# Kernel optimization log

Hardware: AMD Instinct MI355X
Metric: run time of the kernel (lower is better)

## Reference

```python
import jax, jax.numpy as jnp
import numpy as np

E, K, H, I = 8, 2, 768, 1152  # experts, top_k, hidden, intermediate
T = 4096  # total tokens


def setup_inputs() -> dict:
    key = jax.random.key(0)
    ks = jax.random.split(key, 6)
    return {
        "x": jax.random.normal(ks[0], (T, H), jnp.float32),
        "gate_w": jax.random.normal(ks[1], (E, H), jnp.float32) * 0.02,
        "correction_bias": jnp.zeros((E,), jnp.float32),
        "Wi": jax.random.normal(ks[2], (E, H, 2 * I), jnp.float32) * 0.02,
        "Wo": jax.random.normal(ks[3], (E, I, H), jnp.float32) * 0.02,
        "shared_Wi": jax.random.normal(ks[4], (2 * I, H), jnp.float32) * 0.02,
        "shared_Wo": jax.random.normal(ks[5], (H, I), jnp.float32) * 0.02,
    }


def reference(x, gate_w, correction_bias, Wi, Wo, shared_Wi, shared_Wo):
    # ---- shared SwiGLU expert (dropout=0 in eval) ----
    sh = x @ shared_Wi.T                      # (T, 2I)
    s_in, s_gate = sh[:, :I], sh[:, I:]
    shared_out = (jax.nn.silu(s_in) * s_gate) @ shared_Wo.T  # (T, H)

    # ---- sigmoid top-k router with bias correction ----
    logits = jax.nn.sigmoid(x @ gate_w.T)     # (T, E)
    sel = logits + correction_bias
    _, indices = jax.lax.top_k(sel, K)        # (T, K)
    weights = jnp.take_along_axis(logits, indices, axis=-1)  # bias-free scores
    weights = weights / jnp.sum(weights, axis=-1, keepdims=True)

    # combine weight per (expert, token): cw[e, t] = sum_k weights[t,k]*[indices[t,k]==e]
    one_hot = jax.nn.one_hot(indices, E, dtype=x.dtype)      # (T, K, E)
    cw = jnp.einsum("tke,tk->et", one_hot, weights)          # (E, T)

    # ---- experts: SwiGLU per expert, weighted scatter-combine ----
    h = jnp.einsum("th,ehf->etf", x, Wi)      # (E, T, 2I)
    proj, gate = h[..., :I], h[..., I:]
    act = jax.nn.silu(gate) * proj            # (E, T, I)
    act = act * cw[:, :, None]                # fold combine weights before Wo
    expert_out = jnp.einsum("eti,eih->th", act, Wo)          # (T, H)

    return expert_out + shared_out
```

## Files before the change

### kernel.cpp

```cpp
#include <hip/hip_runtime.h>
#include <stdint.h>

#define E_  8
#define H_  768
#define I_  1152
#define T_  4096
#define F2_ (2*I_)

typedef unsigned short u16;
typedef __attribute__((ext_vector_type(8))) __bf16 bf16x8;
typedef __attribute__((ext_vector_type(4))) float floatx4;

typedef const void __attribute__((address_space(1))) as1_void;
typedef void __attribute__((address_space(3))) as3_void;

__device__ __forceinline__ void gld16(void* lds, const void* g) {
  __builtin_amdgcn_global_load_lds((as1_void*)g, (as3_void*)lds, 16, 0, 0);
}

__device__ __forceinline__ u16 f2bf(float f) {
  union { float f; unsigned int i; } v; v.f = f;
  unsigned int r = v.i + 0x7FFF + ((v.i >> 16) & 1);
  return (u16)(r >> 16);
}

__global__ void convert_two(const float* __restrict__ s1, u16* __restrict__ d1, int n1,
                            const float* __restrict__ s2, u16* __restrict__ d2) {
  int i = (blockIdx.x * 256 + threadIdx.x) * 4;
  const float* s; u16* d;
  if (i < n1) { s = s1 + i; d = d1 + i; }
  else        { s = s2 + (i - n1); d = d2 + (i - n1); }
  float4 v = *(const float4*)s;
  ushort4 u;
  u.x = f2bf(v.x); u.y = f2bf(v.y); u.z = f2bf(v.z); u.w = f2bf(v.w);
  *(ushort4*)d = u;
}

__global__ void transpose_f2b(const float* __restrict__ src, u16* __restrict__ dst,
                              int R, int C) {
  __shared__ u16 tile[64][65];
  const float* s = src + (long)blockIdx.z * R * C;
  u16*         d = dst + (long)blockIdx.z * R * C;
  int r0 = blockIdx.y * 64, c0 = blockIdx.x * 64;
  int tx = threadIdx.x, ty = threadIdx.y;
  #pragma unroll
  for (int k = 0; k < 64; k += 8)
    tile[ty + k][tx] = f2bf(s[(long)(r0 + ty + k) * C + (c0 + tx)]);
  __syncthreads();
  #pragma unroll
  for (int k = 0; k < 64; k += 8)
    d[(long)(c0 + ty + k) * R + (r0 + tx)] = tile[tx][ty + k];
}

__global__ void gate_kernel(const float* __restrict__ x, const float* __restrict__ gw,
                            const float* __restrict__ bias,
                            int* __restrict__ top2e, float* __restrict__ top2w,
                            u16* __restrict__ xb) {
  int t    = blockIdx.x * 4 + (threadIdx.x >> 6);
  int lane = threadIdx.x & 63;
  float acc[E_];
  #pragma unroll
  for (int e = 0; e < E_; e++) acc[e] = 0.f;
  #pragma unroll
  for (int i = 0; i < H_ / 256; i++) {
    int c = i * 256 + lane * 4;
    float4 xv = *(const float4*)(x + (long)t * H_ + c);
    ushort4 u;
    u.x = f2bf(xv.x); u.y = f2bf(xv.y); u.z = f2bf(xv.z); u.w = f2bf(xv.w);
    *(ushort4*)(xb + (long)t * H_ + c) = u;
    #pragma unroll
    for (int e = 0; e < E_; e++) {
      float4 g = *(const float4*)(gw + e * H_ + c);
      acc[e] += xv.x * g.x + xv.y * g.y + xv.z * g.z + xv.w * g.w;
    }
  }
  #pragma unroll
  for (int e = 0; e < E_; e++) {
    #pragma unroll
    for (int s = 32; s > 0; s >>= 1) acc[e] += __shfl_xor(acc[e], s);
  }
  if (lane == 0) {
    float logits[E_], sel[E_];
    #pragma unroll
    for (int e = 0; e < E_; e++) {
      logits[e] = 1.f / (1.f + expf(-acc[e]));
      sel[e]    = logits[e] + bias[e];
    }
    int i0 = 0;
    #pragma unroll
    for (int e = 1; e < E_; e++) if (sel[e] > sel[i0]) i0 = e;
    int i1 = (i0 == 0) ? 1 : 0;
    #pragma unroll
    for (int e = 0; e < E_; e++) if (e != i0 && sel[e] > sel[i1]) i1 = e;
    float w0 = logits[i0], w1 = logits[i1], s = w0 + w1;
    top2e[t * 2 + 0] = i0;  top2w[t * 2 + 0] = w0 / s;
    top2e[t * 2 + 1] = i1;  top2w[t * 2 + 1] = w1 / s;
  }
}

__global__ void build_lists(const int* __restrict__ top2e, const float* __restrict__ top2w,
                            int* __restrict__ counts, int* __restrict__ offs,
                            int* __restrict__ list, float* __restrict__ wlist,
                            int* __restrict__ pos) {
  __shared__ int scnt[4][E_];
  __shared__ int sq[4];
  __shared__ int soffs[E_];
  int e = blockIdx.x;
  int tid = threadIdx.x, w = tid >> 6, lane = tid & 63;
  const int Q = (2 * T_) / 4;

  int c8[E_];
  #pragma unroll
  for (int q = 0; q < E_; q++) c8[q] = 0;
  for (int i = tid; i < 2 * T_; i += 256) {
    int v = top2e[i];
    #pragma unroll
    for (int q = 0; q < E_; q++) c8[q] += (v == q);
  }
  int qstart = w * Q;
  int ce = 0;
  for (int i = qstart + lane; i < qstart + Q; i += 64) ce += (top2e[i] == e);
  #pragma unroll
  for (int q = 0; q < E_; q++)
    #pragma unroll
    for (int s = 32; s > 0; s >>= 1) c8[q] += __shfl_xor(c8[q], s);
  #pragma unroll
  for (int s = 32; s > 0; s >>= 1) ce += __shfl_xor(ce, s);
  if (lane == 0) {
    #pragma unroll
    for (int q = 0; q < E_; q++) scnt[w][q] = c8[q];
    sq[w] = ce;
  }
  __syncthreads();
  if (tid == 0) {
    int s = 0;
    #pragma unroll
    for (int q = 0; q < E_; q++) {
      int tot = scnt[0][q] + scnt[1][q] + scnt[2][q] + scnt[3][q];
      soffs[q] = s;
      if (e == 0) { counts[q] = tot; offs[q] = s; }
      s += tot;
    }
    if (e == 0) { counts[8] = T_; offs[8] = 2 * T_; }
  }
  __syncthreads();
  int base = soffs[e];
  #pragma unroll
  for (int w2 = 0; w2 < 4; w2++) if (w2 < w) base += sq[w2];
  unsigned long long lt = (lane == 63) ? (~0ull >> 1) : ((1ull << lane) - 1);
  for (int i0 = qstart; i0 < qstart + Q; i0 += 64) {
    int s = i0 + lane;
    bool m = (top2e[s] == e);
    unsigned long long mask = __ballot(m);
    if (m) {
      int p = base + __popcll(mask & lt);
      list[p]  = s >> 1;
      wlist[p] = top2w[s];
      pos[s]   = p;
    }
    base += __popcll(mask);
  }
  for (int t = e * (T_ / 8) + tid; t < (e + 1) * (T_ / 8); t += 256) {
    list[2 * T_ + t]  = t;
    wlist[2 * T_ + t] = 1.f;
  }
}

#define PP1 168
__global__ __launch_bounds__(256, 2)
void gemm_act_all(const u16* __restrict__ A, const u16* __restrict__ WiT,
                  const u16* __restrict__ sWib, u16* __restrict__ act,
                  const int* __restrict__ list, const float* __restrict__ wlist,
                  const int* __restrict__ counts, const int* __restrict__ offsets) {
  __shared__ __align__(16) u16 As[128 * 64];
  __shared__ __align__(16) u16 Bs[2][64 * 64];

  int id = blockIdx.x;
  int y  = id / PP1, p = id - y * PP1;
  if (p >= 162) return;
  int z = p / 18, xblk = p - z * 18;

  int cnt = counts[z], off = offsets[z];
  int row0 = y * 128;
  if (row0 >= cnt) return;
  const u16* B = (z == 8) ? sWib : (WiT + (long)z * F2_ * H_);
  int n0 = xblk * 64;

  int tid  = threadIdx.x;
  int lane = tid & 63, wv = tid >> 6;
  int wr   = wv >> 1, wc = wv & 1;
  int half = lane & 15, quad = lane >> 4;

  int rA  = tid >> 3;
  int lc8 = ((tid & 7) ^ (rA & 7)) * 8;
  const u16* ap[4];
  #pragma unroll
  for (int n = 0; n < 4; n++) {
    int rr = min(row0 + rA + n * 32, cnt - 1);
    ap[n] = A + (long)list[off + rr] * H_ + lc8;
  }
  const u16* bp[2][2];
  #pragma unroll
  for (int h = 0; h < 2; h++)
    #pragma unroll
    for (int m = 0; m < 2; m++)
      bp[h][m] = B + (long)(h * I_ + n0 + m * 32 + rA) * H_ + lc8;

  floatx4 acc[2][4][2];
  #pragma unroll
  for (int q = 0; q < 2; q++)
    #pragma unroll
    for (int i = 0; i < 4; i++)
      #pragma unroll
      for (int j = 0; j < 2; j++) acc[q][i][j] = (floatx4)0.f;

  for (int k0 = 0; k0 < H_; k0 += 64) {
    if (k0) __syncthreads();
    #pragma unroll
    for (int n = 0; n < 4; n++) gld16(As + (n * 256 + tid) * 8, ap[n] + k0);
    #pragma unroll
    for (int h = 0; h < 2; h++)
      #pragma unroll
      for (int m = 0; m < 2; m++) gld16(Bs[h] + (m * 256 + tid) * 8, bp[h][m] + k0);
    __syncthreads();
    #pragma unroll
    for (int kk = 0; kk < 2; kk++) {
      int cs = ((kk * 4 + quad) ^ (half & 7)) * 8;
      bf16x8 a[4], bq[2][2];
      #pragma unroll
      for (int i = 0; i < 4; i++)
        a[i] = *(const bf16x8*)(As + (wr * 64 + i * 16 + half) * 64 + cs);
      #pragma unroll
      for (int q = 0; q < 2; q++)
        #pragma unroll
        for (int j = 0; j < 2; j++)
          bq[q][j] = *(const bf16x8*)(Bs[q] + (wc * 32 + j * 16 + half) * 64 + cs);
      #pragma unroll
      for (int i = 0; i < 4; i++)
        #pragma unroll
        for (int q = 0; q < 2; q++)
          #pragma unroll
          for (int j = 0; j < 2; j++)
            acc[q][i][j] = __builtin_amdgcn_mfma_f32_16x16x32_bf16(a[i], bq[q][j], acc[q][i][j], 0, 0, 0);
    }
  }

  bool sh = (z == 8);
  #pragma unroll
  for (int i = 0; i < 4; i++) {
    #pragma unroll
    for (int r = 0; r < 4; r++) {
      int g = row0 + wr * 64 + i * 16 + quad * 4 + r;
      if (g < cnt) {
        float w = wlist[off + g];
        #pragma unroll
        for (int j = 0; j < 2; j++) {
          float va = acc[0][i][j][r];
          float vb = acc[1][i][j][r];
          float zz = sh ? va : vb;
          float o  = sh ? vb : va;
          float sg = zz / (1.f + expf(-zz));
          float v  = sg * o * w;
          int col  = n0 + wc * 32 + j * 16 + half;
          act[(long)(off + g) * I_ + col] = f2bf(v);
        }
      }
    }
  }
}

#define PP2 56
__global__ __launch_bounds__(256, 2)
void gemm_out_all(const u16* __restrict__ A, const u16* __restrict__ WoT,
                  const u16* __restrict__ sWob, float* __restrict__ out,
                  float* __restrict__ eobuf,
                  const int* __restrict__ counts, const int* __restrict__ offsets) {
  __shared__ __align__(16) u16 As[128 * 64];
  __shared__ __align__(16) u16 Bs[128 * 64];

  int id = blockIdx.x;
  int y  = id / PP2, p = id - y * PP2;
  if (p >= 54) return;
  int z = p / 6, xblk = p - z * 6;

  int cnt = counts[z], off = offsets[z];
  int row0 = y * 128;
  if (row0 >= cnt) return;
  const u16* B = (z == 8) ? sWob : (WoT + (long)z * H_ * I_);
  int n0 = xblk * 128;

  int tid  = threadIdx.x;
  int lane = tid & 63, wv = tid >> 6;
  int wr   = wv >> 1, wc = wv & 1;
  int half = lane & 15, quad = lane >> 4;

  int rA  = tid >> 3;
  int lc8 = ((tid & 7) ^ (rA & 7)) * 8;
  const u16* ap[4];
  #pragma unroll
  for (int n = 0; n < 4; n++) {
    long rr = off + min(row0 + rA + n * 32, cnt - 1);
    ap[n] = A + rr * I_ + lc8;
  }
  const u16* bp[4];
  #pragma unroll
  for (int m = 0; m < 4; m++)
    bp[m] = B + (long)(n0 + m * 32 + rA) * I_ + lc8;

  floatx4 acc[4][4];
  #pragma unroll
  for (int i = 0; i < 4; i++)
    #pragma unroll
    for (int j = 0; j < 4; j++) acc[i][j] = (floatx4)0.f;

  for (int k0 = 0; k0 < I_; k0 += 64) {
    if (k0) __syncthreads();
    #pragma unroll
    for (int n = 0; n < 4; n++) gld16(As + (n * 256 + tid) * 8, ap[n] + k0);
    #pragma unroll
    for (int m = 0; m < 4; m++) gld16(Bs + (m * 256 + tid) * 8, bp[m] + k0);
    __syncthreads();
    #pragma unroll
    for (int kk = 0; kk < 2; kk++) {
      int cs = ((kk * 4 + quad) ^ (half & 7)) * 8;
      bf16x8 a[4], b[4];
      #pragma unroll
      for (int i = 0; i < 4; i++)
        a[i] = *(const bf16x8*)(As + (wr * 64 + i * 16 + half) * 64 + cs);
      #pragma unroll
      for (int j = 0; j < 4; j++)
        b[j] = *(const bf16x8*)(Bs + (wc * 64 + j * 16 + half) * 64 + cs);
      #pragma unroll
      for (int i = 0; i < 4; i++)
        #pragma unroll
        for (int j = 0; j < 4; j++)
          acc[i][j] = __builtin_amdgcn_mfma_f32_16x16x32_bf16(a[i], b[j], acc[i][j], 0, 0, 0);
    }
  }

  bool sh = (z == 8);
  #pragma unroll
  for (int i = 0; i < 4; i++) {
    #pragma unroll
    for (int r = 0; r < 4; r++) {
      int g = row0 + wr * 64 + i * 16 + quad * 4 + r;
      if (g < cnt) {
        float* orow = sh ? (out + (long)g * H_) : (eobuf + (long)(off + g) * H_);
        #pragma unroll
        for (int j = 0; j < 4; j++) {
          int col = n0 + wc * 64 + j * 16 + half;
          orow[col] = acc[i][j][r];
        }
      }
    }
  }
}

__global__ void final_reduce(float* __restrict__ out, const float* __restrict__ eobuf,
                             const int* __restrict__ pos) {
  int gid = blockIdx.x * 256 + threadIdx.x;
  int t = gid / (H_ / 4), c = (gid % (H_ / 4)) * 4;
  int p0 = pos[t * 2], p1 = pos[t * 2 + 1];
  float4 a = *(const float4*)(out   + (long)t  * H_ + c);
  float4 b = *(const float4*)(eobuf + (long)p0 * H_ + c);
  float4 d = *(const float4*)(eobuf + (long)p1 * H_ + c);
  a.x += b.x + d.x; a.y += b.y + d.y; a.z += b.z + d.z; a.w += b.w + d.w;
  *(float4*)(out + (long)t * H_ + c) = a;
}

extern "C" void kernel_launch(void* const* d_in, const int* in_sizes, int n_in,
                              void* d_out, int out_size, void* d_ws, size_t ws_size,
                              hipStream_t stream) {
  const float* x      = (const float*)d_in[0];
  const float* gate_w = (const float*)d_in[1];
  const float* bias   = (const float*)d_in[2];
  const float* Wi     = (const float*)d_in[3];
  const float* Wo     = (const float*)d_in[4];
  const float* sWi    = (const float*)d_in[5];
  const float* sWo    = (const float*)d_in[6];
  float* out          = (float*)d_out;

  char* ws = (char*)d_ws;
  size_t o = 0;
  auto alloc = [&](size_t bytes) -> void* {
    o = (o + 255) & ~(size_t)255;
    void* p = ws + o;
    o += bytes;
    return p;
  };
  u16*   xb    = (u16*)  alloc((size_t)T_ * H_ * 2);
  u16*   sWib  = (u16*)  alloc((size_t)F2_ * H_ * 2);
  u16*   sWob  = (u16*)  alloc((size_t)H_ * I_ * 2);
  u16*   WiT   = (u16*)  alloc((size_t)E_ * F2_ * H_ * 2);
  u16*   WoT   = (u16*)  alloc((size_t)E_ * H_ * I_ * 2);
  u16*   act   = (u16*)  alloc((size_t)3 * T_ * I_ * 2);
  int*   top2e = (int*)  alloc((size_t)T_ * 2 * 4);
  float* top2w = (float*)alloc((size_t)T_ * 2 * 4);
  int*   count = (int*)  alloc(9 * 4);
  int*   offs  = (int*)  alloc(9 * 4);
  int*   list  = (int*)  alloc((size_t)3 * T_ * 4);
  float* wlist = (float*)alloc((size_t)3 * T_ * 4);
  int*   pos   = (int*)  alloc((size_t)2 * T_ * 4);
  float* eobuf = (float*)WiT;

  gate_kernel<<<T_ / 4, 256, 0, stream>>>(x, gate_w, bias, top2e, top2w, xb);
  build_lists<<<E_, 256, 0, stream>>>(top2e, top2w, count, offs, list, wlist, pos);

  convert_two<<<(F2_ * H_ + H_ * I_) / 1024, 256, 0, stream>>>(
      sWi, sWib, F2_ * H_, sWo, sWob);
  transpose_f2b<<<dim3(F2_ / 64, H_ / 64, E_), dim3(64, 8), 0, stream>>>(Wi, WiT, H_, F2_);
  transpose_f2b<<<dim3(H_ / 64, I_ / 64, E_), dim3(64, 8), 0, stream>>>(Wo, WoT, I_, H_);

  gemm_act_all<<<32 * PP1, 256, 0, stream>>>(xb, WiT, sWib, act, list, wlist, count, offs);
  gemm_out_all<<<32 * PP2, 256, 0, stream>>>(act, WoT, sWob, out, eobuf, count, offs);
  final_reduce<<<(T_ * (H_ / 4)) / 256, 256, 0, stream>>>(out, eobuf, pos);
}
```

Measured before the change: 300.2 us.

## Double-buffer LDS tiles in both expert GEMM kernels to overlap loads with MFMA

Both grouped GEMM kernels now use two LDS buffers for the A and B tiles. The async global-to-LDS loads for the next K-slab are issued before the MFMA work on the current slab, and there is one barrier per slab instead of two. The aim is to hide global memory latency behind compute. In exchange, LDS use per block doubles, which could limit occupancy, and each barrier still waits for all outstanding loads to finish.

```diff
diff --git a/kernel.cpp b/kernel.cpp
--- a/kernel.cpp
+++ b/kernel.cpp
@@ -172,8 +172,10 @@
                   const u16* __restrict__ sWib, u16* __restrict__ act,
                   const int* __restrict__ list, const float* __restrict__ wlist,
                   const int* __restrict__ counts, const int* __restrict__ offsets) {
-  __shared__ __align__(16) u16 As[128 * 64];
-  __shared__ __align__(16) u16 Bs[2][64 * 64];
+  __shared__ __align__(16) u16 As0[128 * 64];
+  __shared__ __align__(16) u16 As1[128 * 64];
+  __shared__ __align__(16) u16 Bs0[2 * 64 * 64];
+  __shared__ __align__(16) u16 Bs1[2 * 64 * 64];
 
   int id = blockIdx.x;
   int y  = id / PP1, p = id - y * PP1;
@@ -214,27 +216,28 @@
       #pragma unroll
       for (int j = 0; j < 2; j++) acc[q][i][j] = (floatx4)0.f;
 
-  for (int k0 = 0; k0 < H_; k0 += 64) {
-    if (k0) __syncthreads();
-    #pragma unroll
-    for (int n = 0; n < 4; n++) gld16(As + (n * 256 + tid) * 8, ap[n] + k0);
-    #pragma unroll
-    for (int h = 0; h < 2; h++)
-      #pragma unroll
-      for (int m = 0; m < 2; m++) gld16(Bs[h] + (m * 256 + tid) * 8, bp[h][m] + k0);
-    __syncthreads();
+  auto stage = [&](u16* as, u16* bs, int k0) {
+    #pragma unroll
+    for (int n = 0; n < 4; n++) gld16(as + (n * 256 + tid) * 8, ap[n] + k0);
+    #pragma unroll
+    for (int h2 = 0; h2 < 2; h2++)
+      #pragma unroll
+      for (int m = 0; m < 2; m++)
+        gld16(bs + h2 * 4096 + (m * 256 + tid) * 8, bp[h2][m] + k0);
+  };
+  auto compute = [&](const u16* as, const u16* bs) {
     #pragma unroll
     for (int kk = 0; kk < 2; kk++) {
       int cs = ((kk * 4 + quad) ^ (half & 7)) * 8;
       bf16x8 a[4], bq[2][2];
       #pragma unroll
       for (int i = 0; i < 4; i++)
-        a[i] = *(const bf16x8*)(As + (wr * 64 + i * 16 + half) * 64 + cs);
+        a[i] = *(const bf16x8*)(as + (wr * 64 + i * 16 + half) * 64 + cs);
       #pragma unroll
       for (int q = 0; q < 2; q++)
         #pragma unroll
         for (int j = 0; j < 2; j++)
-          bq[q][j] = *(const bf16x8*)(Bs[q] + (wc * 32 + j * 16 + half) * 64 + cs);
+          bq[q][j] = *(const bf16x8*)(bs + q * 4096 + (wc * 32 + j * 16 + half) * 64 + cs);
       #pragma unroll
       for (int i = 0; i < 4; i++)
         #pragma unroll
@@ -243,6 +246,17 @@
           for (int j = 0; j < 2; j++)
             acc[q][i][j] = __builtin_amdgcn_mfma_f32_16x16x32_bf16(a[i], bq[q][j], acc[q][i][j], 0, 0, 0);
     }
+  };
+
+  stage(As0, Bs0, 0);
+  __syncthreads();
+  for (int k0 = 0; k0 < H_; k0 += 128) {
+    stage(As1, Bs1, k0 + 64);
+    compute(As0, Bs0);
+    __syncthreads();
+    if (k0 + 128 < H_) stage(As0, Bs0, k0 + 128);
+    compute(As1, Bs1);
+    if (k0 + 128 < H_) __syncthreads();
   }
 
   bool sh = (z == 8);
@@ -275,8 +289,10 @@
                   const u16* __restrict__ sWob, float* __restrict__ out,
                   float* __restrict__ eobuf,
                   const int* __restrict__ counts, const int* __restrict__ offsets) {
-  __shared__ __align__(16) u16 As[128 * 64];
-  __shared__ __align__(16) u16 Bs[128 * 64];
+  __shared__ __align__(16) u16 As0[128 * 64];
+  __shared__ __align__(16) u16 As1[128 * 64];
+  __shared__ __align__(16) u16 Bs0[128 * 64];
+  __shared__ __align__(16) u16 Bs1[128 * 64];
 
   int id = blockIdx.x;
   int y  = id / PP2, p = id - y * PP2;
@@ -313,29 +329,40 @@
     #pragma unroll
     for (int j = 0; j < 4; j++) acc[i][j] = (floatx4)0.f;
 
-  for (int k0 = 0; k0 < I_; k0 += 64) {
-    if (k0) __syncthreads();
-    #pragma unroll
-    for (int n = 0; n < 4; n++) gld16(As + (n * 256 + tid) * 8, ap[n] + k0);
-    #pragma unroll
-    for (int m = 0; m < 4; m++) gld16(Bs + (m * 256 + tid) * 8, bp[m] + k0);
-    __syncthreads();
+  auto stage = [&](u16* as, u16* bs, int k0) {
+    #pragma unroll
+    for (int n = 0; n < 4; n++) gld16(as + (n * 256 + tid) * 8, ap[n] + k0);
+    #pragma unroll
+    for (int m = 0; m < 4; m++) gld16(bs + (m * 256 + tid) * 8, bp[m] + k0);
+  };
+  auto compute = [&](const u16* as, const u16* bs) {
     #pragma unroll
     for (int kk = 0; kk < 2; kk++) {
       int cs = ((kk * 4 + quad) ^ (half & 7)) * 8;
       bf16x8 a[4], b[4];
       #pragma unroll
       for (int i = 0; i < 4; i++)
-        a[i] = *(const bf16x8*)(As + (wr * 64 + i * 16 + half) * 64 + cs);
+        a[i] = *(const bf16x8*)(as + (wr * 64 + i * 16 + half) * 64 + cs);
       #pragma unroll
       for (int j = 0; j < 4; j++)
-        b[j] = *(const bf16x8*)(Bs + (wc * 64 + j * 16 + half) * 64 + cs);
+        b[j] = *(const bf16x8*)(bs + (wc * 64 + j * 16 + half) * 64 + cs);
       #pragma unroll
       for (int i = 0; i < 4; i++)
         #pragma unroll
         for (int j = 0; j < 4; j++)
           acc[i][j] = __builtin_amdgcn_mfma_f32_16x16x32_bf16(a[i], b[j], acc[i][j], 0, 0, 0);
     }
+  };
+
+  stage(As0, Bs0, 0);
+  __syncthreads();
+  for (int k0 = 0; k0 < I_; k0 += 128) {
+    stage(As1, Bs1, k0 + 64);
+    compute(As0, Bs0);
+    __syncthreads();
+    if (k0 + 128 < I_) stage(As0, Bs0, k0 + 128);
+    compute(As1, Bs1);
+    if (k0 + 128 < I_) __syncthreads();
   }
 
   bool sh = (z == 8);
```

New measurement: 306.7 us. 1.02x slower.

## Fuse prep kernels into one launch, reorder GEMM block mapping, shrink out-GEMM tile

Applied to the files above, without the earlier changes.

Merges the gate/routing, shared-weight conversion and the two expert weight transposes into one prep_all kernel that dispatches on block index. This removes three launches and lets independent prep work share the GPU. Both GEMMs now put the row-block index in the low bits of the block id, so consecutive blocks share the same weight columns. gemm_out_all uses 64-row tiles with occupancy hint 4, which doubles its grid for better load balance at the cost of more reloads of the B tiles.

```diff
diff --git a/kernel.cpp b/kernel.cpp
--- a/kernel.cpp
+++ b/kernel.cpp
@@ -24,77 +24,101 @@
   return (u16)(r >> 16);
 }
 
-__global__ void convert_two(const float* __restrict__ s1, u16* __restrict__ d1, int n1,
-                            const float* __restrict__ s2, u16* __restrict__ d2) {
-  int i = (blockIdx.x * 256 + threadIdx.x) * 4;
-  const float* s; u16* d;
-  if (i < n1) { s = s1 + i; d = d1 + i; }
-  else        { s = s2 + (i - n1); d = d2 + (i - n1); }
-  float4 v = *(const float4*)s;
-  ushort4 u;
-  u.x = f2bf(v.x); u.y = f2bf(v.y); u.z = f2bf(v.z); u.w = f2bf(v.w);
-  *(ushort4*)d = u;
-}
-
-__global__ void transpose_f2b(const float* __restrict__ src, u16* __restrict__ dst,
-                              int R, int C) {
+#define GATE_BLKS (T_ / 4)
+#define CONV_BLKS ((F2_ * H_ + H_ * I_) / 1024)
+#define TWI_X (F2_ / 64)
+#define TWI_Y (H_ / 64)
+#define TWI_BLKS (TWI_X * TWI_Y * E_)
+#define TWO_X (H_ / 64)
+#define TWO_Y (I_ / 64)
+#define TWO_BLKS (TWO_X * TWO_Y * E_)
+#define PREP_BLKS (GATE_BLKS + CONV_BLKS + TWI_BLKS + TWO_BLKS)
+
+__device__ __forceinline__ void transpose_role(const float* __restrict__ src,
+                                               u16* __restrict__ dst,
+                                               int R, int C, int xi, int yi, int zi) {
   __shared__ u16 tile[64][65];
-  const float* s = src + (long)blockIdx.z * R * C;
-  u16*         d = dst + (long)blockIdx.z * R * C;
-  int r0 = blockIdx.y * 64, c0 = blockIdx.x * 64;
-  int tx = threadIdx.x, ty = threadIdx.y;
-  #pragma unroll
-  for (int k = 0; k < 64; k += 8)
+  const float* s = src + (long)zi * R * C;
+  u16*         d = dst + (long)zi * R * C;
+  int r0 = yi * 64, c0 = xi * 64;
+  int tx = threadIdx.x & 63, ty = threadIdx.x >> 6;
+  #pragma unroll
+  for (int k = 0; k < 64; k += 4)
     tile[ty + k][tx] = f2bf(s[(long)(r0 + ty + k) * C + (c0 + tx)]);
   __syncthreads();
   #pragma unroll
-  for (int k = 0; k < 64; k += 8)
+  for (int k = 0; k < 64; k += 4)
     d[(long)(c0 + ty + k) * R + (r0 + tx)] = tile[tx][ty + k];
 }
 
-__global__ void gate_kernel(const float* __restrict__ x, const float* __restrict__ gw,
-                            const float* __restrict__ bias,
-                            int* __restrict__ top2e, float* __restrict__ top2w,
-                            u16* __restrict__ xb) {
-  int t    = blockIdx.x * 4 + (threadIdx.x >> 6);
-  int lane = threadIdx.x & 63;
-  float acc[E_];
-  #pragma unroll
-  for (int e = 0; e < E_; e++) acc[e] = 0.f;
-  #pragma unroll
-  for (int i = 0; i < H_ / 256; i++) {
-    int c = i * 256 + lane * 4;
-    float4 xv = *(const float4*)(x + (long)t * H_ + c);
+__global__ __launch_bounds__(256)
+void prep_all(const float* __restrict__ x, const float* __restrict__ gw,
+              const float* __restrict__ bias,
+              int* __restrict__ top2e, float* __restrict__ top2w, u16* __restrict__ xb,
+              const float* __restrict__ sWi, u16* __restrict__ sWib,
+              const float* __restrict__ sWo, u16* __restrict__ sWob,
+              const float* __restrict__ Wi, u16* __restrict__ WiT,
+              const float* __restrict__ Wo, u16* __restrict__ WoT) {
+  int b = blockIdx.x;
+  if (b < GATE_BLKS) {
+    int t    = b * 4 + (threadIdx.x >> 6);
+    int lane = threadIdx.x & 63;
+    float acc[E_];
+    #pragma unroll
+    for (int e = 0; e < E_; e++) acc[e] = 0.f;
+    #pragma unroll
+    for (int i = 0; i < H_ / 256; i++) {
+      int c = i * 256 + lane * 4;
+      float4 xv = *(const float4*)(x + (long)t * H_ + c);
+      ushort4 u;
+      u.x = f2bf(xv.x); u.y = f2bf(xv.y); u.z = f2bf(xv.z); u.w = f2bf(xv.w);
+      *(ushort4*)(xb + (long)t * H_ + c) = u;
+      #pragma unroll
+      for (int e = 0; e < E_; e++) {
+        float4 g = *(const float4*)(gw + e * H_ + c);
+        acc[e] += xv.x * g.x + xv.y * g.y + xv.z * g.z + xv.w * g.w;
+      }
+    }
+    #pragma unroll
+    for (int e = 0; e < E_; e++) {
+      #pragma unroll
+      for (int s = 32; s > 0; s >>= 1) acc[e] += __shfl_xor(acc[e], s);
+    }
+    if (lane == 0) {
+      float logits[E_], sel[E_];
+      #pragma unroll
+      for (int e = 0; e < E_; e++) {
+        logits[e] = 1.f / (1.f + expf(-acc[e]));
+        sel[e]    = logits[e] + bias[e];
+      }
+      int i0 = 0;
+      #pragma unroll
+      for (int e = 1; e < E_; e++) if (sel[e] > sel[i0]) i0 = e;
+      int i1 = (i0 == 0) ? 1 : 0;
+      #pragma unroll
+      for (int e = 0; e < E_; e++) if (e != i0 && sel[e] > sel[i1]) i1 = e;
+      float w0 = logits[i0], w1 = logits[i1], s = w0 + w1;
+      top2e[t * 2 + 0] = i0;  top2w[t * 2 + 0] = w0 / s;
+      top2e[t * 2 + 1] = i1;  top2w[t * 2 + 1] = w1 / s;
+    }
+  } else if (b < GATE_BLKS + CONV_BLKS) {
+    int i = ((b - GATE_BLKS) * 256 + threadIdx.x) * 4;
+    const int n1 = F2_ * H_;
+    const float* s; u16* d;
+    if (i < n1) { s = sWi + i; d = sWib + i; }
+    else        { s = sWo + (i - n1); d = sWob + (i - n1); }
+    float4 v = *(const float4*)s;
     ushort4 u;
-    u.x = f2bf(xv.x); u.y = f2bf(xv.y); u.z = f2bf(xv.z); u.w = f2bf(xv.w);
-    *(ushort4*)(xb + (long)t * H_ + c) = u;
-    #pragma unroll
-    for (int e = 0; e < E_; e++) {
-      float4 g = *(const float4*)(gw + e * H_ + c);
-      acc[e] += xv.x * g.x + xv.y * g.y + xv.z * g.z + xv.w * g.w;
-    }
-  }
-  #pragma unroll
-  for (int e = 0; e < E_; e++) {
-    #pragma unroll
-    for (int s = 32; s > 0; s >>= 1) acc[e] += __shfl_xor(acc[e], s);
-  }
-  if (lane == 0) {
-    float logits[E_], sel[E_];
-    #pragma unroll
-    for (int e = 0; e < E_; e++) {
-      logits[e] = 1.f / (1.f + expf(-acc[e]));
-      sel[e]    = logits[e] + bias[e];
-    }
-    int i0 = 0;
-    #pragma unroll
-    for (int e = 1; e < E_; e++) if (sel[e] > sel[i0]) i0 = e;
-    int i1 = (i0 == 0) ? 1 : 0;
-    #pragma unroll
-    for (int e = 0; e < E_; e++) if (e != i0 && sel[e] > sel[i1]) i1 = e;
-    float w0 = logits[i0], w1 = logits[i1], s = w0 + w1;
-    top2e[t * 2 + 0] = i0;  top2w[t * 2 + 0] = w0 / s;
-    top2e[t * 2 + 1] = i1;  top2w[t * 2 + 1] = w1 / s;
+    u.x = f2bf(v.x); u.y = f2bf(v.y); u.z = f2bf(v.z); u.w = f2bf(v.w);
+    *(ushort4*)d = u;
+  } else if (b < GATE_BLKS + CONV_BLKS + TWI_BLKS) {
+    int i = b - (GATE_BLKS + CONV_BLKS);
+    int xi = i % TWI_X, yi = (i / TWI_X) % TWI_Y, zi = i / (TWI_X * TWI_Y);
+    transpose_role(Wi, WiT, H_, F2_, xi, yi, zi);
+  } else {
+    int i = b - (GATE_BLKS + CONV_BLKS + TWI_BLKS);
+    int xi = i % TWO_X, yi = (i / TWO_X) % TWO_Y, zi = i / (TWO_X * TWO_Y);
+    transpose_role(Wo, WoT, I_, H_, xi, yi, zi);
   }
 }
 
@@ -176,7 +200,7 @@
   __shared__ __align__(16) u16 Bs[2][64 * 64];
 
   int id = blockIdx.x;
-  int y  = id / PP1, p = id - y * PP1;
+  int y  = id & 31, p = id >> 5;
   if (p >= 162) return;
   int z = p / 18, xblk = p - z * 18;
 
@@ -270,21 +294,21 @@
 }
 
 #define PP2 56
-__global__ __launch_bounds__(256, 2)
+__global__ __launch_bounds__(256, 4)
 void gemm_out_all(const u16* __restrict__ A, const u16* __restrict__ WoT,
                   const u16* __restrict__ sWob, float* __restrict__ out,
                   float* __restrict__ eobuf,
                   const int* __restrict__ counts, const int* __restrict__ offsets) {
-  __shared__ __align__(16) u16 As[128 * 64];
+  __shared__ __align__(16) u16 As[64 * 64];
   __shared__ __align__(16) u16 Bs[128 * 64];
 
   int id = blockIdx.x;
-  int y  = id / PP2, p = id - y * PP2;
+  int y  = id & 63, p = id >> 6;
   if (p >= 54) return;
   int z = p / 6, xblk = p - z * 6;
 
   int cnt = counts[z], off = offsets[z];
-  int row0 = y * 128;
+  int row0 = y * 64;
   if (row0 >= cnt) return;
   const u16* B = (z == 8) ? sWob : (WoT + (long)z * H_ * I_);
   int n0 = xblk * 128;
@@ -296,9 +320,9 @@
 
   int rA  = tid >> 3;
   int lc8 = ((tid & 7) ^ (rA & 7)) * 8;
-  const u16* ap[4];
-  #pragma unroll
-  for (int n = 0; n < 4; n++) {
+  const u16* ap[2];
+  #pragma unroll
+  for (int n = 0; n < 2; n++) {
     long rr = off + min(row0 + rA + n * 32, cnt - 1);
     ap[n] = A + rr * I_ + lc8;
   }
@@ -307,31 +331,31 @@
   for (int m = 0; m < 4; m++)
     bp[m] = B + (long)(n0 + m * 32 + rA) * I_ + lc8;
 
-  floatx4 acc[4][4];
-  #pragma unroll
-  for (int i = 0; i < 4; i++)
+  floatx4 acc[2][4];
+  #pragma unroll
+  for (int i = 0; i < 2; i++)
     #pragma unroll
     for (int j = 0; j < 4; j++) acc[i][j] = (floatx4)0.f;
 
   for (int k0 = 0; k0 < I_; k0 += 64) {
     if (k0) __syncthreads();
     #pragma unroll
-    for (int n = 0; n < 4; n++) gld16(As + (n * 256 + tid) * 8, ap[n] + k0);
+    for (int n = 0; n < 2; n++) gld16(As + (n * 256 + tid) * 8, ap[n] + k0);
     #pragma unroll
     for (int m = 0; m < 4; m++) gld16(Bs + (m * 256 + tid) * 8, bp[m] + k0);
     __syncthreads();
     #pragma unroll
     for (int kk = 0; kk < 2; kk++) {
       int cs = ((kk * 4 + quad) ^ (half & 7)) * 8;
-      bf16x8 a[4], b[4];
-      #pragma unroll
-      for (int i = 0; i < 4; i++)
-        a[i] = *(const bf16x8*)(As + (wr * 64 + i * 16 + half) * 64 + cs);
+      bf16x8 a[2], b[4];
+      #pragma unroll
+      for (int i = 0; i < 2; i++)
+        a[i] = *(const bf16x8*)(As + (wr * 32 + i * 16 + half) * 64 + cs);
       #pragma unroll
       for (int j = 0; j < 4; j++)
         b[j] = *(const bf16x8*)(Bs + (wc * 64 + j * 16 + half) * 64 + cs);
       #pragma unroll
-      for (int i = 0; i < 4; i++)
+      for (int i = 0; i < 2; i++)
         #pragma unroll
         for (int j = 0; j < 4; j++)
           acc[i][j] = __builtin_amdgcn_mfma_f32_16x16x32_bf16(a[i], b[j], acc[i][j], 0, 0, 0);
@@ -340,10 +364,10 @@
 
   bool sh = (z == 8);
   #pragma unroll
-  for (int i = 0; i < 4; i++) {
+  for (int i = 0; i < 2; i++) {
     #pragma unroll
     for (int r = 0; r < 4; r++) {
-      int g = row0 + wr * 64 + i * 16 + quad * 4 + r;
+      int g = row0 + wr * 32 + i * 16 + quad * 4 + r;
       if (g < cnt) {
         float* orow = sh ? (out + (long)g * H_) : (eobuf + (long)(off + g) * H_);
         #pragma unroll
@@ -403,15 +427,11 @@
   int*   pos   = (int*)  alloc((size_t)2 * T_ * 4);
   float* eobuf = (float*)WiT;
 
-  gate_kernel<<<T_ / 4, 256, 0, stream>>>(x, gate_w, bias, top2e, top2w, xb);
+  prep_all<<<PREP_BLKS, 256, 0, stream>>>(x, gate_w, bias, top2e, top2w, xb,
+                                          sWi, sWib, sWo, sWob, Wi, WiT, Wo, WoT);
   build_lists<<<E_, 256, 0, stream>>>(top2e, top2w, count, offs, list, wlist, pos);
 
-  convert_two<<<(F2_ * H_ + H_ * I_) / 1024, 256, 0, stream>>>(
-      sWi, sWib, F2_ * H_, sWo, sWob);
-  transpose_f2b<<<dim3(F2_ / 64, H_ / 64, E_), dim3(64, 8), 0, stream>>>(Wi, WiT, H_, F2_);
-  transpose_f2b<<<dim3(H_ / 64, I_ / 64, E_), dim3(64, 8), 0, stream>>>(Wo, WoT, I_, H_);
-
   gemm_act_all<<<32 * PP1, 256, 0, stream>>>(xb, WiT, sWib, act, list, wlist, count, offs);
-  gemm_out_all<<<32 * PP2, 256, 0, stream>>>(act, WoT, sWob, out, eobuf, count, offs);
+  gemm_out_all<<<64 * PP2, 256, 0, stream>>>(act, WoT, sWob, out, eobuf, count, offs);
   final_reduce<<<(T_ * (H_ / 4)) / 256, 256, 0, stream>>>(out, eobuf, pos);
 }
```

Measured after the change: 364.2 us. +21.3%, slower.
